# Kernel tuning notes

Measured on AMD Instinct MI355X. Metric: run time of the kernel, lower is better.

Reference implementation:

```python
import jax, jax.numpy as jnp
import numpy as np

B, L, D = 1, 2048, 2048
NH, NKV, HD = 32, 8, 64          # heads, kv heads, head_dim = D // NH
THETA = 50000.0
EPS = 1e-5
SCALE = HD ** -0.5


def _rope(x):
    # traditional (interleaved-pair) RoPE; x: (B, H, L, HD)
    hd = x.shape[-1]
    pos = jnp.arange(x.shape[2], dtype=jnp.float32)
    inv = THETA ** (-jnp.arange(0, hd, 2, dtype=jnp.float32) / hd)
    ang = pos[:, None] * inv[None, :]              # (L, HD/2)
    cos, sin = jnp.cos(ang), jnp.sin(ang)
    x1, x2 = x[..., ::2], x[..., 1::2]
    r1 = x1 * cos - x2 * sin
    r2 = x1 * sin + x2 * cos
    return jnp.stack([r1, r2], axis=-1).reshape(x.shape)


def _rmsnorm(x, w):
    return x * jax.lax.rsqrt(jnp.mean(x * x, axis=-1, keepdims=True) + EPS) * w


def setup_inputs() -> dict:
    key = jax.random.key(0)
    ks = jax.random.split(key, 5)
    x = jax.random.normal(ks[0], (B, L, D), dtype=jnp.float32)
    w_qkv = jax.random.normal(ks[1], (NH * HD + 2 * NKV * HD, D), dtype=jnp.float32) * 0.02
    w_out = jax.random.normal(ks[2], (D, D), dtype=jnp.float32) * 0.02
    q_gamma = 1.0 + 0.02 * jax.random.normal(ks[3], (HD,), dtype=jnp.float32)
    k_gamma = 1.0 + 0.02 * jax.random.normal(ks[4], (HD,), dtype=jnp.float32)
    mask = jnp.tril(jnp.ones((L, L), dtype=bool))   # causal
    return {"x": x, "w_qkv": w_qkv, "w_out": w_out,
            "q_gamma": q_gamma, "k_gamma": k_gamma, "mask": mask}


def reference(x, w_qkv, w_out, q_gamma, k_gamma, mask):
    b, l, d = x.shape
    qkv = x @ w_qkv.T                               # fused QKV proj (no bias)
    q, k, v = jnp.split(qkv, [NH * HD, NH * HD + NKV * HD], axis=-1)
    q = q.reshape(b, l, NH, HD).transpose(0, 2, 1, 3)     # (B,NH,L,HD)
    k = k.reshape(b, l, NKV, HD).transpose(0, 2, 1, 3)    # (B,NKV,L,HD)
    v = v.reshape(b, l, NKV, HD).transpose(0, 2, 1, 3)
    q = _rmsnorm(_rope(q), q_gamma)
    k = _rmsnorm(_rope(k), k_gamma)
    g = NH // NKV                                   # GQA group size
    qg = q.reshape(b, NKV, g, l, HD)
    scores = jnp.einsum('bkgqd,bkld->bkgql', qg, k) * SCALE
    scores = jnp.where(mask, scores, -jnp.inf)
    attn = jax.nn.softmax(scores, axis=-1)
    out = jnp.einsum('bkgql,bkld->bkgqd', attn, v)  # (B,NKV,g,L,HD)
    out = out.reshape(b, NH, l, HD).transpose(0, 2, 1, 3).reshape(b, l, d)
    return out @ w_out.T
```

## Files before the change

kernel.cpp:

```cpp
#include <hip/hip_runtime.h>

using bf16   = __bf16;
using bf16x4 = __bf16 __attribute__((ext_vector_type(4)));
using bf16x8 = __bf16 __attribute__((ext_vector_type(8)));
using f32x4  = float __attribute__((ext_vector_type(4)));
using f32x16 = float __attribute__((ext_vector_type(16)));
using u32x2  = unsigned int __attribute__((ext_vector_type(2)));
using u32x4  = unsigned int __attribute__((ext_vector_type(4)));

#define L_SEQ  2048
#define DMODEL 2048
#define NQH    32
#define NKVH   8
#define HDIM   64
#define QKV_N  3072

#define KVF_HSTRIDE (64 * 4 * 64 * 8)

__device__ __forceinline__ void gload_lds16(const void* g, void* lds) {
  __builtin_amdgcn_global_load_lds((__attribute__((address_space(1))) void*)(g),
                                   (__attribute__((address_space(3))) void*)(lds),
                                   16, 0, 0);
}

__device__ __forceinline__ unsigned pack2(float a, float b) {
  union { bf16 h[2]; unsigned u; } x;
  x.h[0] = (bf16)a; x.h[1] = (bf16)b;
  return x.u;
}

__device__ __forceinline__ bf16x8 make_pfrag(float p0, float p1, float p2, float p3,
                                             float p4, float p5, float p6, float p7,
                                             int hi) {
  const unsigned W0 = pack2(p0, p1);
  const unsigned W1 = pack2(p2, p3);
  const unsigned W2 = pack2(p4, p5);
  const unsigned W3 = pack2(p6, p7);
  u32x4 pw;
#if __has_builtin(__builtin_amdgcn_permlane32_swap)
  {
    using i32x2 = int __attribute__((ext_vector_type(2)));
    const i32x2 r02 = __builtin_amdgcn_permlane32_swap((int)W0, (int)W2, false, false);
    const i32x2 r13 = __builtin_amdgcn_permlane32_swap((int)W1, (int)W3, false, false);
    pw = u32x4{ (unsigned)r02[0], (unsigned)r13[0], (unsigned)r02[1], (unsigned)r13[1] };
  }
#else
  {
    const unsigned X0 = (unsigned)__shfl_xor((int)W0, 32);
    const unsigned X1 = (unsigned)__shfl_xor((int)W1, 32);
    const unsigned X2 = (unsigned)__shfl_xor((int)W2, 32);
    const unsigned X3 = (unsigned)__shfl_xor((int)W3, 32);
    pw = u32x4{ hi ? X2 : W0, hi ? X3 : W1, hi ? W2 : X0, hi ? W3 : X1 };
  }
#endif
  return __builtin_bit_cast(bf16x8, pw);
}

__device__ __forceinline__ int chunk_base(int qi) {
  return (qi < 16) ? qi
       : (qi < 32) ? 16 + 2 * (qi - 16)
       : (qi < 48) ? 48 + 3 * (qi - 32)
                   : 96 + 4 * (qi - 48);
}

#define N4_X  (L_SEQ * DMODEL / 4)
#define N4_WQ (QKV_N * DMODEL / 4)
#define N4_WO (DMODEL * DMODEL / 4)
__global__ void cvt3_f32_bf16(const float* __restrict__ x, const float* __restrict__ wq,
                              const float* __restrict__ wo, bf16* __restrict__ xb,
                              bf16* __restrict__ wqb, bf16* __restrict__ wob) {
  const long stride = (long)gridDim.x * blockDim.x;
  const long ntot = N4_X + N4_WQ + N4_WO;
  for (long i = (long)blockIdx.x * blockDim.x + threadIdx.x; i < ntot; i += stride) {
    const float* src; bf16* dst; long j;
    if (i < N4_X)               { src = x;  dst = xb;  j = i; }
    else if (i < N4_X + N4_WQ)  { src = wq; dst = wqb; j = i - N4_X; }
    else                        { src = wo; dst = wob; j = i - N4_X - N4_WQ; }
    const float4 v = reinterpret_cast<const float4*>(src)[j];
    bf16x4 o = { (bf16)v.x, (bf16)v.y, (bf16)v.z, (bf16)v.w };
    reinterpret_cast<bf16x4*>(dst)[j] = o;
  }
}

template <typename OutT>
__global__ __launch_bounds__(128)
void gemm_bt(const bf16* __restrict__ A, const bf16* __restrict__ B,
             OutT* __restrict__ C, int M, int N, int K) {
  __shared__ bf16 As[128 * 64];
  __shared__ bf16 Bs[64 * 64];
  const int tid = threadIdx.x;
  const int w = tid >> 6, l = tid & 63;
  const int lq = l & 15, lg = l >> 4;
  const long m0 = (long)blockIdx.y * 128;
  const long n0 = (long)blockIdx.x * 64;
  const int ks = K / gridDim.z;
  const int kb = blockIdx.z * ks;
  C += (long)blockIdx.z * M * N;

  const int lrow = l >> 3;
  const int scol = ((l & 7) ^ lrow) << 3;

  f32x4 acc[4][4];
#pragma unroll
  for (int i = 0; i < 4; ++i)
#pragma unroll
    for (int j = 0; j < 4; ++j) acc[i][j] = f32x4{0.f, 0.f, 0.f, 0.f};

  for (int k0 = kb; k0 < kb + ks; k0 += 64) {
#pragma unroll
    for (int i = 0; i < 8; ++i) {
      const int r0 = (i * 2 + w) * 8;
      gload_lds16(A + (m0 + r0 + lrow) * (long)K + k0 + scol, &As[r0 * 64]);
    }
#pragma unroll
    for (int i = 0; i < 4; ++i) {
      const int r0 = (i * 2 + w) * 8;
      gload_lds16(B + (n0 + r0 + lrow) * (long)K + k0 + scol, &Bs[r0 * 64]);
    }
    __syncthreads();
#pragma unroll
    for (int kk = 0; kk < 2; ++kk) {
      bf16x8 af[4], bfr[4];
#pragma unroll
      for (int t = 0; t < 4; ++t) {
        const int rowA = w * 64 + t * 16 + lq;
        const int blkA = (kk * 4 + lg) ^ (rowA & 7);
        af[t] = *reinterpret_cast<const bf16x8*>(&As[rowA * 64 + blkA * 8]);
        const int rowB = t * 16 + lq;
        const int blkB = (kk * 4 + lg) ^ (rowB & 7);
        bfr[t] = *reinterpret_cast<const bf16x8*>(&Bs[rowB * 64 + blkB * 8]);
      }
#pragma unroll
      for (int mt = 0; mt < 4; ++mt)
#pragma unroll
        for (int nt = 0; nt < 4; ++nt)
          acc[mt][nt] = __builtin_amdgcn_mfma_f32_16x16x32_bf16(af[mt], bfr[nt], acc[mt][nt], 0, 0, 0);
    }
    __syncthreads();
  }

#pragma unroll
  for (int mt = 0; mt < 4; ++mt)
#pragma unroll
    for (int r = 0; r < 4; ++r) {
      const long row = m0 + w * 64 + mt * 16 + lg * 4 + r;
#pragma unroll
      for (int nt = 0; nt < 4; ++nt) {
        const long col = n0 + nt * 16 + lq;
        C[row * (long)N + col] = (OutT)acc[mt][nt][r];
      }
    }
}

__global__ __launch_bounds__(256)
void rope_rms(const bf16* __restrict__ pA, const bf16* __restrict__ pB,
              const float* __restrict__ qg, const float* __restrict__ kg,
              bf16* __restrict__ qo, bf16* __restrict__ kfr) {
  const int gid = blockIdx.x * 4 + (threadIdx.x >> 6);
  const int lane = threadIdx.x & 63;
  const int pos = gid / 40;
  const int hh = gid % 40;
  const bool isq = hh < 32;
  const int col = isq ? hh * HDIM : NQH * HDIM + (hh - 32) * HDIM;

  const long idx = (long)pos * QKV_N + col + lane;
  float x = (float)pA[idx] + (float)pB[idx];
  float p = __shfl_xor(x, 1);
  const float fi = (float)(lane & ~1) * (1.0f / 64.0f);
  const float inv = powf(50000.0f, -fi);
  const float ang = (float)pos * inv;
  const float sn = sinf(ang), cs = cosf(ang);
  const float r = (lane & 1) ? (p * sn + x * cs) : (x * cs - p * sn);

  float ss = r * r;
#pragma unroll
  for (int off = 1; off < 64; off <<= 1) ss += __shfl_xor(ss, off);
  const float scl = rsqrtf(ss * (1.0f / 64.0f) + 1e-5f);
  const float g = isq ? qg[lane] : kg[lane];
  const float o = r * scl * g;

  if (isq) {
    qo[(long)pos * DMODEL + hh * HDIM + lane] = (bf16)(o * 0.18033688011112042f);
  } else {
    const int kvh = hh - 32;
    const int d = lane;
    const int lp = (pos & 31) + (((d >> 3) & 1) << 5);
    const long kidx = ((((long)kvh * 64 + (pos >> 5)) * 4 + (d >> 4)) * 64 + lp) * 8 + (d & 7);
    kfr[kidx] = (bf16)o;
  }
}

__global__ __launch_bounds__(256)
void repack_v(const bf16* __restrict__ pA, const bf16* __restrict__ pB,
              bf16* __restrict__ vfr) {
  __shared__ bf16 t[32][72];
  const int kvh = blockIdx.x >> 6;
  const int kb = blockIdx.x & 63;
  const int tid = threadIdx.x;

  {
    const int row = tid >> 3;
    const int cc = (tid & 7) * 8;
    const long goff = (long)(kb * 32 + row) * QKV_N + (NQH * HDIM + NKVH * HDIM) + kvh * HDIM + cc;
    const bf16x8 a = *reinterpret_cast<const bf16x8*>(pA + goff);
    const bf16x8 b = *reinterpret_cast<const bf16x8*>(pB + goff);
    bf16x8 s;
#pragma unroll
    for (int e = 0; e < 8; ++e) s[e] = (bf16)((float)a[e] + (float)b[e]);
    *reinterpret_cast<bf16x8*>(&t[row][cc]) = s;
  }
  __syncthreads();

  const int f = tid >> 6, l = tid & 63;
  const int s = f >> 1, dh = f & 1;
  const int hi = l >> 5, l31 = l & 31;
  union { bf16 b[8]; u32x4 u; } o;
#pragma unroll
  for (int e = 0; e < 8; ++e) o.b[e] = t[s * 16 + hi * 8 + e][dh * 32 + l31];
  bf16* od = vfr + (((long)(kvh * 64 + kb) * 4 + f) * 64 + l) * 8;
  *reinterpret_cast<u32x4*>(od) = o.u;
}

__global__ __launch_bounds__(256)
void flash_attn(const bf16* __restrict__ Q, const bf16* __restrict__ Kfr,
                const bf16* __restrict__ Vfr,
                bf16* __restrict__ po, float* __restrict__ pm, float* __restrict__ pl) {
  const int w = threadIdx.x >> 6, l = threadIdx.x & 63;
  const int lane31 = l & 31, hi = l >> 5;
  const int bb = blockIdx.x;
  const int kvh = bb & 7;
  const int g = bb >> 3;

  int qi, c;
  if (g < 16)      { qi = g;                  c = 0; }
  else if (g < 48) { qi = 16 + ((g - 16) >> 1); c = (g - 16) & 1; }
  else if (g < 96) { qi = 32 + (g - 48) / 3;    c = (g - 48) % 3; }
  else             { qi = 48 + ((g - 96) >> 2); c = (g - 96) & 3; }

  const int h = kvh * 4 + w;
  const int s0 = c * 16;
  const int s1 = min(qi + 1, s0 + 16);
  const int pidx = h * 160 + g;

  const int q0 = qi * 32;
  const int q_abs = q0 + lane31;
  const int l8 = l * 8;

  const bf16* qrow = Q + (long)q_abs * DMODEL + h * HDIM + hi * 8;
  bf16x8 qf[4];
#pragma unroll
  for (int cc = 0; cc < 4; ++cc) qf[cc] = *reinterpret_cast<const bf16x8*>(qrow + cc * 16);

  f32x16 o0, o1;
#pragma unroll
  for (int r = 0; r < 16; ++r) { o0[r] = 0.f; o1[r] = 0.f; }
  float m = -3.0e38f, lsum = 0.f;

  const bf16* kfrh = Kfr + (long)kvh * KVF_HSTRIDE;
  const bf16* vfrh = Vfr + (long)kvh * KVF_HSTRIDE;

  bf16x8 kc0, kc1, kc2, kc3;
  {
    const bf16* kp = kfrh + (long)s0 * 2048 + l8;
    kc0 = *reinterpret_cast<const bf16x8*>(kp);
    kc1 = *reinterpret_cast<const bf16x8*>(kp + 512);
    kc2 = *reinterpret_cast<const bf16x8*>(kp + 1024);
    kc3 = *reinterpret_cast<const bf16x8*>(kp + 1536);
  }

  for (int sti = s0; sti < s1; ++sti) {
    const int kb0 = sti * 32;

    const bf16* vp = vfrh + (long)sti * 2048 + l8;
    const bf16x8 va0 = *reinterpret_cast<const bf16x8*>(vp);
    const bf16x8 vb0 = *reinterpret_cast<const bf16x8*>(vp + 512);
    const bf16x8 va1 = *reinterpret_cast<const bf16x8*>(vp + 1024);
    const bf16x8 vb1 = *reinterpret_cast<const bf16x8*>(vp + 1536);

    const long knoff = (sti + 1 < s1) ? (long)(sti + 1) * 2048 : (long)s0 * 2048;
    const bf16* kp = kfrh + knoff + l8;
    const bf16x8 kn0 = *reinterpret_cast<const bf16x8*>(kp);
    const bf16x8 kn1 = *reinterpret_cast<const bf16x8*>(kp + 512);
    const bf16x8 kn2 = *reinterpret_cast<const bf16x8*>(kp + 1024);
    const bf16x8 kn3 = *reinterpret_cast<const bf16x8*>(kp + 1536);

    f32x16 st;
#pragma unroll
    for (int r = 0; r < 16; ++r) st[r] = 0.f;
    st = __builtin_amdgcn_mfma_f32_32x32x16_bf16(kc0, qf[0], st, 0, 0, 0);
    st = __builtin_amdgcn_mfma_f32_32x32x16_bf16(kc1, qf[1], st, 0, 0, 0);
    st = __builtin_amdgcn_mfma_f32_32x32x16_bf16(kc2, qf[2], st, 0, 0, 0);
    st = __builtin_amdgcn_mfma_f32_32x32x16_bf16(kc3, qf[3], st, 0, 0, 0);

    if (kb0 + 31 > q0) {
#pragma unroll
      for (int r = 0; r < 16; ++r) {
        const int k_abs = kb0 + (r & 3) + 8 * (r >> 2) + 4 * hi;
        if (k_abs > q_abs) st[r] = -3.0e38f;
      }
    }

    float t[8];
#pragma unroll
    for (int r = 0; r < 8; ++r) t[r] = fmaxf(st[r], st[r + 8]);
#pragma unroll
    for (int s = 4; s > 0; s >>= 1)
#pragma unroll
      for (int r = 0; r < 4; ++r) if (r < s) t[r] = fmaxf(t[r], t[r + s]);
    float mx = fmaxf(t[0], __shfl_xor(t[0], 32));

    if (!__all(mx - m <= 8.0f)) {
      const float mn = fmaxf(m, mx);
      const float al = __builtin_amdgcn_exp2f(m - mn);
      m = mn; lsum *= al;
#pragma unroll
      for (int r = 0; r < 16; ++r) { o0[r] *= al; o1[r] *= al; }
    }
    float rs = 0.f;
#pragma unroll
    for (int r = 0; r < 16; ++r) { st[r] = __builtin_amdgcn_exp2f(st[r] - m); rs += st[r]; }
    rs += __shfl_xor(rs, 32);
    lsum += rs;

    {
      const bf16x8 pf0 = make_pfrag(st[0], st[1], st[2], st[3], st[4], st[5], st[6], st[7], hi);
      o0 = __builtin_amdgcn_mfma_f32_32x32x16_bf16(va0, pf0, o0, 0, 0, 0);
      o1 = __builtin_amdgcn_mfma_f32_32x32x16_bf16(vb0, pf0, o1, 0, 0, 0);
      const bf16x8 pf1 = make_pfrag(st[8], st[9], st[10], st[11], st[12], st[13], st[14], st[15], hi);
      o0 = __builtin_amdgcn_mfma_f32_32x32x16_bf16(va1, pf1, o0, 0, 0, 0);
      o1 = __builtin_amdgcn_mfma_f32_32x32x16_bf16(vb1, pf1, o1, 0, 0, 0);
    }

    kc0 = kn0; kc1 = kn1; kc2 = kn2; kc3 = kn3;
  }

  bf16* pbase = po + (long)pidx * 2048 + lane31 * 64;
#pragma unroll
  for (int gg = 0; gg < 4; ++gg) {
    const int d0 = 8 * gg + 4 * hi;
    u32x2 s0v = { pack2(o0[4 * gg + 0], o0[4 * gg + 1]),
                  pack2(o0[4 * gg + 2], o0[4 * gg + 3]) };
    u32x2 s1v = { pack2(o1[4 * gg + 0], o1[4 * gg + 1]),
                  pack2(o1[4 * gg + 2], o1[4 * gg + 3]) };
    *reinterpret_cast<u32x2*>(pbase + d0) = s0v;
    *reinterpret_cast<u32x2*>(pbase + 32 + d0) = s1v;
  }
  if (hi == 0) {
    pm[pidx * 32 + lane31] = m;
    pl[pidx * 32 + lane31] = lsum;
  }
}

__global__ __launch_bounds__(256)
void combine_split(const bf16* __restrict__ po, const float* __restrict__ pm,
                   const float* __restrict__ pl, bf16* __restrict__ ao) {
  const int t = blockIdx.x * 2 + (threadIdx.x >> 7);
  const int tid7 = threadIdx.x & 127;
  const int r = tid7 >> 2;
  const int dc = (tid7 & 3) * 16;
  const int h = t >> 6, qi = t & 63;
  const int nc = 1 + (qi >> 4);
  const int p0 = h * 160 + chunk_base(qi);

  float mv0 = -3e38f, mv1 = -3e38f, mv2 = -3e38f, mv3 = -3e38f;
  float lv0 = 0.f, lv1 = 0.f, lv2 = 0.f, lv3 = 0.f;
  mv0 = pm[(p0 + 0) * 32 + r];              lv0 = pl[(p0 + 0) * 32 + r];
  if (nc > 1) { mv1 = pm[(p0 + 1) * 32 + r]; lv1 = pl[(p0 + 1) * 32 + r]; }
  if (nc > 2) { mv2 = pm[(p0 + 2) * 32 + r]; lv2 = pl[(p0 + 2) * 32 + r]; }
  if (nc > 3) { mv3 = pm[(p0 + 3) * 32 + r]; lv3 = pl[(p0 + 3) * 32 + r]; }
  const float M = fmaxf(fmaxf(mv0, mv1), fmaxf(mv2, mv3));
  const float w0 = __builtin_amdgcn_exp2f(mv0 - M);
  const float w1 = (nc > 1) ? __builtin_amdgcn_exp2f(mv1 - M) : 0.f;
  const float w2 = (nc > 2) ? __builtin_amdgcn_exp2f(mv2 - M) : 0.f;
  const float w3 = (nc > 3) ? __builtin_amdgcn_exp2f(mv3 - M) : 0.f;
  const float invL = 1.0f / (lv0 * w0 + lv1 * w1 + lv2 * w2 + lv3 * w3);

  float acc[16];
#pragma unroll
  for (int j = 0; j < 16; ++j) acc[j] = 0.f;

#pragma unroll
  for (int c = 0; c < 4; ++c) {
    if (c < nc) {
      const float fc = ((c == 0) ? w0 : (c == 1) ? w1 : (c == 2) ? w2 : w3) * invL;
      const bf16* src = po + ((long)(p0 + c) * 2048) + r * 64 + dc;
      const bf16x8 a0 = *reinterpret_cast<const bf16x8*>(src);
      const bf16x8 a1 = *reinterpret_cast<const bf16x8*>(src + 8);
#pragma unroll
      for (int j = 0; j < 8; ++j) {
        acc[j]     += (float)a0[j] * fc;
        acc[8 + j] += (float)a1[j] * fc;
      }
    }
  }

  const long q_abs = (long)qi * 32 + r;
  bf16* od = ao + q_abs * DMODEL + h * HDIM + dc;
  union { bf16 b[16]; u32x4 u[2]; } o;
#pragma unroll
  for (int j = 0; j < 16; ++j) o.b[j] = (bf16)acc[j];
  *reinterpret_cast<u32x4*>(od) = o.u[0];
  *reinterpret_cast<u32x4*>(od + 8) = o.u[1];
}

extern "C" void kernel_launch(void* const* d_in, const int* in_sizes, int n_in,
                              void* d_out, int out_size, void* d_ws, size_t ws_size,
                              hipStream_t stream) {
  const float* x       = (const float*)d_in[0];
  const float* w_qkv   = (const float*)d_in[1];
  const float* w_out   = (const float*)d_in[2];
  const float* q_gamma = (const float*)d_in[3];
  const float* k_gamma = (const float*)d_in[4];

  char* ws = (char*)d_ws;
  bf16* xb    = (bf16*)(ws);
  bf16* wqb   = (bf16*)(ws + (8ul  << 20));
  bf16* wob   = (bf16*)(ws + (20ul << 20));
  bf16* qkvpA = (bf16*)(ws + (28ul << 20));
  bf16* qkvpB = (bf16*)(ws + (40ul << 20));
  bf16* qb    = (bf16*)(ws);
  bf16* kfr   = (bf16*)(ws + (8ul  << 20));
  bf16* vfr   = (bf16*)(ws + (10ul << 20));
  bf16* po    = (bf16*)(ws + (28ul << 20));
  float* pm   = (float*)(ws + (48ul << 20));
  float* pl   = (float*)(ws + (49ul << 20));
  bf16* ao    = (bf16*)(ws + (52ul << 20));
  float* out  = (float*)d_out;

  cvt3_f32_bf16<<<2048, 256, 0, stream>>>(x, w_qkv, w_out, xb, wqb, wob);

  gemm_bt<bf16><<<dim3(QKV_N / 64, L_SEQ / 128, 2), 128, 0, stream>>>(xb, wqb, qkvpA, L_SEQ, QKV_N, DMODEL);

  rope_rms<<<(L_SEQ * 40) / 4, 256, 0, stream>>>(qkvpA, qkvpB, q_gamma, k_gamma, qb, kfr);
  repack_v<<<NKVH * (L_SEQ / 32), 256, 0, stream>>>(qkvpA, qkvpB, vfr);

  flash_attn<<<1280, 256, 0, stream>>>(qb, kfr, vfr, po, pm, pl);
  combine_split<<<1024, 256, 0, stream>>>(po, pm, pl, ao);

  gemm_bt<float><<<dim3(DMODEL / 64, L_SEQ / 128, 1), 128, 0, stream>>>(ao, wob, out, L_SEQ, DMODEL, DMODEL);
}
```

Before: 168.9 us.

## Stage K/V tiles through double-buffered LDS via async global-to-LDS loads

Previously each of the four waves loaded the same K and V fragments straight from global memory into registers. Now the block loads each K/V tile into shared memory once, using async global_load_lds, with double buffering. Each wave then reads its fragments from LDS, which is meant to cut redundant global/L2 traffic by about 4x. The cost is a block-wide barrier every iteration and an LDS read step on the critical path.

```diff
diff --git a/kernel.cpp b/kernel.cpp
--- a/kernel.cpp
+++ b/kernel.cpp
@@ -225,7 +225,10 @@
 void flash_attn(const bf16* __restrict__ Q, const bf16* __restrict__ Kfr,
                 const bf16* __restrict__ Vfr,
                 bf16* __restrict__ po, float* __restrict__ pm, float* __restrict__ pl) {
-  const int w = threadIdx.x >> 6, l = threadIdx.x & 63;
+  __shared__ bf16 Ks[2][2048];
+  __shared__ bf16 Vs[2][2048];
+  const int tid = threadIdx.x;
+  const int w = tid >> 6, l = tid & 63;
   const int lane31 = l & 31, hi = l >> 5;
   const int bb = blockIdx.x;
   const int kvh = bb & 7;
@@ -246,6 +249,9 @@
   const int q_abs = q0 + lane31;
   const int l8 = l * 8;
 
+  const bf16* kfrh = Kfr + (long)kvh * KVF_HSTRIDE;
+  const bf16* vfrh = Vfr + (long)kvh * KVF_HSTRIDE;
+
   const bf16* qrow = Q + (long)q_abs * DMODEL + h * HDIM + hi * 8;
   bf16x8 qf[4];
 #pragma unroll
@@ -256,34 +262,23 @@
   for (int r = 0; r < 16; ++r) { o0[r] = 0.f; o1[r] = 0.f; }
   float m = -3.0e38f, lsum = 0.f;
 
-  const bf16* kfrh = Kfr + (long)kvh * KVF_HSTRIDE;
-  const bf16* vfrh = Vfr + (long)kvh * KVF_HSTRIDE;
-
-  bf16x8 kc0, kc1, kc2, kc3;
-  {
-    const bf16* kp = kfrh + (long)s0 * 2048 + l8;
-    kc0 = *reinterpret_cast<const bf16x8*>(kp);
-    kc1 = *reinterpret_cast<const bf16x8*>(kp + 512);
-    kc2 = *reinterpret_cast<const bf16x8*>(kp + 1024);
-    kc3 = *reinterpret_cast<const bf16x8*>(kp + 1536);
-  }
-
+  gload_lds16(kfrh + (long)s0 * 2048 + tid * 8, &Ks[0][tid * 8]);
+  gload_lds16(vfrh + (long)s0 * 2048 + tid * 8, &Vs[0][tid * 8]);
+  __syncthreads();
+
+  int buf = 0;
   for (int sti = s0; sti < s1; ++sti) {
     const int kb0 = sti * 32;
 
-    const bf16* vp = vfrh + (long)sti * 2048 + l8;
-    const bf16x8 va0 = *reinterpret_cast<const bf16x8*>(vp);
-    const bf16x8 vb0 = *reinterpret_cast<const bf16x8*>(vp + 512);
-    const bf16x8 va1 = *reinterpret_cast<const bf16x8*>(vp + 1024);
-    const bf16x8 vb1 = *reinterpret_cast<const bf16x8*>(vp + 1536);
-
-    const long knoff = (sti + 1 < s1) ? (long)(sti + 1) * 2048 : (long)s0 * 2048;
-    const bf16* kp = kfrh + knoff + l8;
-    const bf16x8 kn0 = *reinterpret_cast<const bf16x8*>(kp);
-    const bf16x8 kn1 = *reinterpret_cast<const bf16x8*>(kp + 512);
-    const bf16x8 kn2 = *reinterpret_cast<const bf16x8*>(kp + 1024);
-    const bf16x8 kn3 = *reinterpret_cast<const bf16x8*>(kp + 1536);
-
+    if (sti + 1 < s1) {
+      gload_lds16(kfrh + (long)(sti + 1) * 2048 + tid * 8, &Ks[buf ^ 1][tid * 8]);
+      gload_lds16(vfrh + (long)(sti + 1) * 2048 + tid * 8, &Vs[buf ^ 1][tid * 8]);
+    }
+
+    const bf16x8 kc0 = *reinterpret_cast<const bf16x8*>(&Ks[buf][l8]);
+    const bf16x8 kc1 = *reinterpret_cast<const bf16x8*>(&Ks[buf][512 + l8]);
+    const bf16x8 kc2 = *reinterpret_cast<const bf16x8*>(&Ks[buf][1024 + l8]);
+    const bf16x8 kc3 = *reinterpret_cast<const bf16x8*>(&Ks[buf][1536 + l8]);
     f32x16 st;
 #pragma unroll
     for (int r = 0; r < 16; ++r) st[r] = 0.f;
@@ -291,6 +286,11 @@
     st = __builtin_amdgcn_mfma_f32_32x32x16_bf16(kc1, qf[1], st, 0, 0, 0);
     st = __builtin_amdgcn_mfma_f32_32x32x16_bf16(kc2, qf[2], st, 0, 0, 0);
     st = __builtin_amdgcn_mfma_f32_32x32x16_bf16(kc3, qf[3], st, 0, 0, 0);
+
+    const bf16x8 va0 = *reinterpret_cast<const bf16x8*>(&Vs[buf][l8]);
+    const bf16x8 vb0 = *reinterpret_cast<const bf16x8*>(&Vs[buf][512 + l8]);
+    const bf16x8 va1 = *reinterpret_cast<const bf16x8*>(&Vs[buf][1024 + l8]);
+    const bf16x8 vb1 = *reinterpret_cast<const bf16x8*>(&Vs[buf][1536 + l8]);
 
     if (kb0 + 31 > q0) {
 #pragma unroll
@@ -331,7 +331,8 @@
       o1 = __builtin_amdgcn_mfma_f32_32x32x16_bf16(vb1, pf1, o1, 0, 0, 0);
     }
 
-    kc0 = kn0; kc1 = kn1; kc2 = kn2; kc3 = kn3;
+    __syncthreads();
+    buf ^= 1;
   }
 
   bf16* pbase = po + (long)pidx * 2048 + lane31 * 64;
```

Result: slower. 172.8 us (+2.3%).

## Process two 32-row query tiles per wave to reuse K/V fragments

Applied to the files above, without the earlier changes.

Each wave in the flash attention kernel now handles 64 query rows, as two 32-row tiles, instead of 32. Every loaded K/V fragment therefore feeds two QK and PV MFMA chains, which halves K/V global traffic per unit of work and halves the grid to 640 blocks. The block order is reversed so the heaviest, most-split causal tiles launch first, and launch_bounds is set to 2 blocks per SM. The combine kernel and the partial-result layout are changed to 64-row chunks. The cost is higher register pressure from four accumulators and fewer blocks to balance the load.

```diff
diff --git a/kernel.cpp b/kernel.cpp
--- a/kernel.cpp
+++ b/kernel.cpp
@@ -56,11 +56,11 @@
   return __builtin_bit_cast(bf16x8, pw);
 }
 
-__device__ __forceinline__ int chunk_base(int qi) {
-  return (qi < 16) ? qi
-       : (qi < 32) ? 16 + 2 * (qi - 16)
-       : (qi < 48) ? 48 + 3 * (qi - 32)
-                   : 96 + 4 * (qi - 48);
+__device__ __forceinline__ int chunk_base64(int Qb) {
+  return (Qb < 8)  ? Qb
+       : (Qb < 16) ? 8  + 2 * (Qb - 8)
+       : (Qb < 24) ? 24 + 3 * (Qb - 16)
+                   : 48 + 4 * (Qb - 24);
 }
 
 #define N4_X  (L_SEQ * DMODEL / 4)
@@ -221,7 +221,7 @@
   *reinterpret_cast<u32x4*>(od) = o.u;
 }
 
-__global__ __launch_bounds__(256)
+__global__ __launch_bounds__(256, 2)
 void flash_attn(const bf16* __restrict__ Q, const bf16* __restrict__ Kfr,
                 const bf16* __restrict__ Vfr,
                 bf16* __restrict__ po, float* __restrict__ pm, float* __restrict__ pl) {
@@ -229,35 +229,40 @@
   const int lane31 = l & 31, hi = l >> 5;
   const int bb = blockIdx.x;
   const int kvh = bb & 7;
-  const int g = bb >> 3;
-
-  int qi, c;
-  if (g < 16)      { qi = g;                  c = 0; }
-  else if (g < 48) { qi = 16 + ((g - 16) >> 1); c = (g - 16) & 1; }
-  else if (g < 96) { qi = 32 + (g - 48) / 3;    c = (g - 48) % 3; }
-  else             { qi = 48 + ((g - 96) >> 2); c = (g - 96) & 3; }
+  const int g = 79 - (bb >> 3);
+
+  int Qb, c;
+  if (g < 8)       { Qb = g;                   c = 0; }
+  else if (g < 24) { Qb = 8 + ((g - 8) >> 1);  c = (g - 8) & 1; }
+  else if (g < 48) { Qb = 16 + (g - 24) / 3;   c = (g - 24) % 3; }
+  else             { Qb = 24 + ((g - 48) >> 2); c = (g - 48) & 3; }
 
   const int h = kvh * 4 + w;
   const int s0 = c * 16;
-  const int s1 = min(qi + 1, s0 + 16);
-  const int pidx = h * 160 + g;
-
-  const int q0 = qi * 32;
-  const int q_abs = q0 + lane31;
+  const int s1 = min(2 * Qb + 2, s0 + 16);
+  const int pidx = h * 80 + g;
+
+  const int q0A = Qb * 64;
+  const int qA = q0A + lane31;
+  const int qB = q0A + 32 + lane31;
   const int l8 = l * 8;
-
-  const bf16* qrow = Q + (long)q_abs * DMODEL + h * HDIM + hi * 8;
-  bf16x8 qf[4];
-#pragma unroll
-  for (int cc = 0; cc < 4; ++cc) qf[cc] = *reinterpret_cast<const bf16x8*>(qrow + cc * 16);
-
-  f32x16 o0, o1;
-#pragma unroll
-  for (int r = 0; r < 16; ++r) { o0[r] = 0.f; o1[r] = 0.f; }
-  float m = -3.0e38f, lsum = 0.f;
 
   const bf16* kfrh = Kfr + (long)kvh * KVF_HSTRIDE;
   const bf16* vfrh = Vfr + (long)kvh * KVF_HSTRIDE;
+
+  const bf16* qrowA = Q + (long)qA * DMODEL + h * HDIM + hi * 8;
+  const bf16* qrowB = Q + (long)qB * DMODEL + h * HDIM + hi * 8;
+  bf16x8 qfA[4], qfB[4];
+#pragma unroll
+  for (int cc = 0; cc < 4; ++cc) {
+    qfA[cc] = *reinterpret_cast<const bf16x8*>(qrowA + cc * 16);
+    qfB[cc] = *reinterpret_cast<const bf16x8*>(qrowB + cc * 16);
+  }
+
+  f32x16 oA0, oA1, oB0, oB1;
+#pragma unroll
+  for (int r = 0; r < 16; ++r) { oA0[r] = 0.f; oA1[r] = 0.f; oB0[r] = 0.f; oB1[r] = 0.f; }
+  float mA = -3.0e38f, lsA = 0.f, mB = -3.0e38f, lsB = 0.f;
 
   bf16x8 kc0, kc1, kc2, kc3;
   {
@@ -284,90 +289,145 @@
     const bf16x8 kn2 = *reinterpret_cast<const bf16x8*>(kp + 1024);
     const bf16x8 kn3 = *reinterpret_cast<const bf16x8*>(kp + 1536);
 
-    f32x16 st;
-#pragma unroll
-    for (int r = 0; r < 16; ++r) st[r] = 0.f;
-    st = __builtin_amdgcn_mfma_f32_32x32x16_bf16(kc0, qf[0], st, 0, 0, 0);
-    st = __builtin_amdgcn_mfma_f32_32x32x16_bf16(kc1, qf[1], st, 0, 0, 0);
-    st = __builtin_amdgcn_mfma_f32_32x32x16_bf16(kc2, qf[2], st, 0, 0, 0);
-    st = __builtin_amdgcn_mfma_f32_32x32x16_bf16(kc3, qf[3], st, 0, 0, 0);
-
-    if (kb0 + 31 > q0) {
-#pragma unroll
-      for (int r = 0; r < 16; ++r) {
-        const int k_abs = kb0 + (r & 3) + 8 * (r >> 2) + 4 * hi;
-        if (k_abs > q_abs) st[r] = -3.0e38f;
-      }
-    }
-
-    float t[8];
-#pragma unroll
-    for (int r = 0; r < 8; ++r) t[r] = fmaxf(st[r], st[r + 8]);
-#pragma unroll
-    for (int s = 4; s > 0; s >>= 1)
-#pragma unroll
-      for (int r = 0; r < 4; ++r) if (r < s) t[r] = fmaxf(t[r], t[r + s]);
-    float mx = fmaxf(t[0], __shfl_xor(t[0], 32));
-
-    if (!__all(mx - m <= 8.0f)) {
-      const float mn = fmaxf(m, mx);
-      const float al = __builtin_amdgcn_exp2f(m - mn);
-      m = mn; lsum *= al;
-#pragma unroll
-      for (int r = 0; r < 16; ++r) { o0[r] *= al; o1[r] *= al; }
-    }
-    float rs = 0.f;
-#pragma unroll
-    for (int r = 0; r < 16; ++r) { st[r] = __builtin_amdgcn_exp2f(st[r] - m); rs += st[r]; }
-    rs += __shfl_xor(rs, 32);
-    lsum += rs;
+    if (kb0 <= q0A + 31) {
+      f32x16 st;
+#pragma unroll
+      for (int r = 0; r < 16; ++r) st[r] = 0.f;
+      st = __builtin_amdgcn_mfma_f32_32x32x16_bf16(kc0, qfA[0], st, 0, 0, 0);
+      st = __builtin_amdgcn_mfma_f32_32x32x16_bf16(kc1, qfA[1], st, 0, 0, 0);
+      st = __builtin_amdgcn_mfma_f32_32x32x16_bf16(kc2, qfA[2], st, 0, 0, 0);
+      st = __builtin_amdgcn_mfma_f32_32x32x16_bf16(kc3, qfA[3], st, 0, 0, 0);
+
+      if (kb0 + 31 > q0A) {
+#pragma unroll
+        for (int r = 0; r < 16; ++r) {
+          const int k_abs = kb0 + (r & 3) + 8 * (r >> 2) + 4 * hi;
+          if (k_abs > qA) st[r] = -3.0e38f;
+        }
+      }
+
+      float t[8];
+#pragma unroll
+      for (int r = 0; r < 8; ++r) t[r] = fmaxf(st[r], st[r + 8]);
+#pragma unroll
+      for (int s = 4; s > 0; s >>= 1)
+#pragma unroll
+        for (int r = 0; r < 4; ++r) if (r < s) t[r] = fmaxf(t[r], t[r + s]);
+      const float mx = fmaxf(t[0], __shfl_xor(t[0], 32));
+
+      if (!__all(mx - mA <= 8.0f)) {
+        const float mn = fmaxf(mA, mx);
+        const float al = __builtin_amdgcn_exp2f(mA - mn);
+        mA = mn; lsA *= al;
+#pragma unroll
+        for (int r = 0; r < 16; ++r) { oA0[r] *= al; oA1[r] *= al; }
+      }
+      float rs = 0.f;
+#pragma unroll
+      for (int r = 0; r < 16; ++r) { st[r] = __builtin_amdgcn_exp2f(st[r] - mA); rs += st[r]; }
+      rs += __shfl_xor(rs, 32);
+      lsA += rs;
+
+      const bf16x8 pf0 = make_pfrag(st[0], st[1], st[2], st[3], st[4], st[5], st[6], st[7], hi);
+      oA0 = __builtin_amdgcn_mfma_f32_32x32x16_bf16(va0, pf0, oA0, 0, 0, 0);
+      oA1 = __builtin_amdgcn_mfma_f32_32x32x16_bf16(vb0, pf0, oA1, 0, 0, 0);
+      const bf16x8 pf1 = make_pfrag(st[8], st[9], st[10], st[11], st[12], st[13], st[14], st[15], hi);
+      oA0 = __builtin_amdgcn_mfma_f32_32x32x16_bf16(va1, pf1, oA0, 0, 0, 0);
+      oA1 = __builtin_amdgcn_mfma_f32_32x32x16_bf16(vb1, pf1, oA1, 0, 0, 0);
+    }
 
     {
+      f32x16 st;
+#pragma unroll
+      for (int r = 0; r < 16; ++r) st[r] = 0.f;
+      st = __builtin_amdgcn_mfma_f32_32x32x16_bf16(kc0, qfB[0], st, 0, 0, 0);
+      st = __builtin_amdgcn_mfma_f32_32x32x16_bf16(kc1, qfB[1], st, 0, 0, 0);
+      st = __builtin_amdgcn_mfma_f32_32x32x16_bf16(kc2, qfB[2], st, 0, 0, 0);
+      st = __builtin_amdgcn_mfma_f32_32x32x16_bf16(kc3, qfB[3], st, 0, 0, 0);
+
+      if (kb0 + 31 > q0A + 32) {
+#pragma unroll
+        for (int r = 0; r < 16; ++r) {
+          const int k_abs = kb0 + (r & 3) + 8 * (r >> 2) + 4 * hi;
+          if (k_abs > qB) st[r] = -3.0e38f;
+        }
+      }
+
+      float t[8];
+#pragma unroll
+      for (int r = 0; r < 8; ++r) t[r] = fmaxf(st[r], st[r + 8]);
+#pragma unroll
+      for (int s = 4; s > 0; s >>= 1)
+#pragma unroll
+        for (int r = 0; r < 4; ++r) if (r < s) t[r] = fmaxf(t[r], t[r + s]);
+      const float mx = fmaxf(t[0], __shfl_xor(t[0], 32));
+
+      if (!__all(mx - mB <= 8.0f)) {
+        const float mn = fmaxf(mB, mx);
+        const float al = __builtin_amdgcn_exp2f(mB - mn);
+        mB = mn; lsB *= al;
+#pragma unroll
+        for (int r = 0; r < 16; ++r) { oB0[r] *= al; oB1[r] *= al; }
+      }
+      float rs = 0.f;
+#pragma unroll
+      for (int r = 0; r < 16; ++r) { st[r] = __builtin_amdgcn_exp2f(st[r] - mB); rs += st[r]; }
+      rs += __shfl_xor(rs, 32);
+      lsB += rs;
+
       const bf16x8 pf0 = make_pfrag(st[0], st[1], st[2], st[3], st[4], st[5], st[6], st[7], hi);
-      o0 = __builtin_amdgcn_mfma_f32_32x32x16_bf16(va0, pf0, o0, 0, 0, 0);
-      o1 = __builtin_amdgcn_mfma_f32_32x32x16_bf16(vb0, pf0, o1, 0, 0, 0);
+      oB0 = __builtin_amdgcn_mfma_f32_32x32x16_bf16(va0, pf0, oB0, 0, 0, 0);
+      oB1 = __builtin_amdgcn_mfma_f32_32x32x16_bf16(vb0, pf0, oB1, 0, 0, 0);
       const bf16x8 pf1 = make_pfrag(st[8], st[9], st[10], st[11], st[12], st[13], st[14], st[15], hi);
-      o0 = __builtin_amdgcn_mfma_f32_32x32x16_bf16(va1, pf1, o0, 0, 0, 0);
-      o1 = __builtin_amdgcn_mfma_f32_32x32x16_bf16(vb1, pf1, o1, 0, 0, 0);
+      oB0 = __builtin_amdgcn_mfma_f32_32x32x16_bf16(va1, pf1, oB0, 0, 0, 0);
+      oB1 = __builtin_amdgcn_mfma_f32_32x32x16_bf16(vb1, pf1, oB1, 0, 0, 0);
     }
 
     kc0 = kn0; kc1 = kn1; kc2 = kn2; kc3 = kn3;
   }
 
-  bf16* pbase = po + (long)pidx * 2048 + lane31 * 64;
+  bf16* pbase = po + (long)pidx * 4096;
 #pragma unroll
   for (int gg = 0; gg < 4; ++gg) {
     const int d0 = 8 * gg + 4 * hi;
-    u32x2 s0v = { pack2(o0[4 * gg + 0], o0[4 * gg + 1]),
-                  pack2(o0[4 * gg + 2], o0[4 * gg + 3]) };
-    u32x2 s1v = { pack2(o1[4 * gg + 0], o1[4 * gg + 1]),
-                  pack2(o1[4 * gg + 2], o1[4 * gg + 3]) };
-    *reinterpret_cast<u32x2*>(pbase + d0) = s0v;
-    *reinterpret_cast<u32x2*>(pbase + 32 + d0) = s1v;
+    u32x2 a0 = { pack2(oA0[4 * gg + 0], oA0[4 * gg + 1]),
+                 pack2(oA0[4 * gg + 2], oA0[4 * gg + 3]) };
+    u32x2 a1 = { pack2(oA1[4 * gg + 0], oA1[4 * gg + 1]),
+                 pack2(oA1[4 * gg + 2], oA1[4 * gg + 3]) };
+    *reinterpret_cast<u32x2*>(pbase + lane31 * 64 + d0) = a0;
+    *reinterpret_cast<u32x2*>(pbase + lane31 * 64 + 32 + d0) = a1;
+    u32x2 b0 = { pack2(oB0[4 * gg + 0], oB0[4 * gg + 1]),
+                 pack2(oB0[4 * gg + 2], oB0[4 * gg + 3]) };
+    u32x2 b1 = { pack2(oB1[4 * gg + 0], oB1[4 * gg + 1]),
+                 pack2(oB1[4 * gg + 2], oB1[4 * gg + 3]) };
+    *reinterpret_cast<u32x2*>(pbase + (32 + lane31) * 64 + d0) = b0;
+    *reinterpret_cast<u32x2*>(pbase + (32 + lane31) * 64 + 32 + d0) = b1;
   }
   if (hi == 0) {
-    pm[pidx * 32 + lane31] = m;
-    pl[pidx * 32 + lane31] = lsum;
+    pm[pidx * 64 + lane31] = mA;
+    pl[pidx * 64 + lane31] = lsA;
+    pm[pidx * 64 + 32 + lane31] = mB;
+    pl[pidx * 64 + 32 + lane31] = lsB;
   }
 }
 
 __global__ __launch_bounds__(256)
 void combine_split(const bf16* __restrict__ po, const float* __restrict__ pm,
                    const float* __restrict__ pl, bf16* __restrict__ ao) {
-  const int t = blockIdx.x * 2 + (threadIdx.x >> 7);
-  const int tid7 = threadIdx.x & 127;
-  const int r = tid7 >> 2;
-  const int dc = (tid7 & 3) * 16;
-  const int h = t >> 6, qi = t & 63;
-  const int nc = 1 + (qi >> 4);
-  const int p0 = h * 160 + chunk_base(qi);
+  const int t = blockIdx.x;
+  const int tid = threadIdx.x;
+  const int r = tid >> 2;
+  const int dc = (tid & 3) * 16;
+  const int h = t >> 5, Qb = t & 31;
+  const int nc = (Qb < 8) ? 1 : (Qb < 16) ? 2 : (Qb < 24) ? 3 : 4;
+  const int p0 = h * 80 + chunk_base64(Qb);
 
   float mv0 = -3e38f, mv1 = -3e38f, mv2 = -3e38f, mv3 = -3e38f;
   float lv0 = 0.f, lv1 = 0.f, lv2 = 0.f, lv3 = 0.f;
-  mv0 = pm[(p0 + 0) * 32 + r];              lv0 = pl[(p0 + 0) * 32 + r];
-  if (nc > 1) { mv1 = pm[(p0 + 1) * 32 + r]; lv1 = pl[(p0 + 1) * 32 + r]; }
-  if (nc > 2) { mv2 = pm[(p0 + 2) * 32 + r]; lv2 = pl[(p0 + 2) * 32 + r]; }
-  if (nc > 3) { mv3 = pm[(p0 + 3) * 32 + r]; lv3 = pl[(p0 + 3) * 32 + r]; }
+  mv0 = pm[(p0 + 0) * 64 + r];              lv0 = pl[(p0 + 0) * 64 + r];
+  if (nc > 1) { mv1 = pm[(p0 + 1) * 64 + r]; lv1 = pl[(p0 + 1) * 64 + r]; }
+  if (nc > 2) { mv2 = pm[(p0 + 2) * 64 + r]; lv2 = pl[(p0 + 2) * 64 + r]; }
+  if (nc > 3) { mv3 = pm[(p0 + 3) * 64 + r]; lv3 = pl[(p0 + 3) * 64 + r]; }
   const float M = fmaxf(fmaxf(mv0, mv1), fmaxf(mv2, mv3));
   const float w0 = __builtin_amdgcn_exp2f(mv0 - M);
   const float w1 = (nc > 1) ? __builtin_amdgcn_exp2f(mv1 - M) : 0.f;
@@ -383,7 +443,7 @@
   for (int c = 0; c < 4; ++c) {
     if (c < nc) {
       const float fc = ((c == 0) ? w0 : (c == 1) ? w1 : (c == 2) ? w2 : w3) * invL;
-      const bf16* src = po + ((long)(p0 + c) * 2048) + r * 64 + dc;
+      const bf16* src = po + ((long)(p0 + c) * 4096) + r * 64 + dc;
       const bf16x8 a0 = *reinterpret_cast<const bf16x8*>(src);
       const bf16x8 a1 = *reinterpret_cast<const bf16x8*>(src + 8);
 #pragma unroll
@@ -394,7 +454,7 @@
     }
   }
 
-  const long q_abs = (long)qi * 32 + r;
+  const long q_abs = (long)Qb * 64 + r;
   bf16* od = ao + q_abs * DMODEL + h * HDIM + dc;
   union { bf16 b[16]; u32x4 u[2]; } o;
 #pragma unroll
@@ -434,7 +494,7 @@
   rope_rms<<<(L_SEQ * 40) / 4, 256, 0, stream>>>(qkvpA, qkvpB, q_gamma, k_gamma, qb, kfr);
   repack_v<<<NKVH * (L_SEQ / 32), 256, 0, stream>>>(qkvpA, qkvpB, vfr);
 
-  flash_attn<<<1280, 256, 0, stream>>>(qb, kfr, vfr, po, pm, pl);
+  flash_attn<<<640, 256, 0, stream>>>(qb, kfr, vfr, po, pm, pl);
   combine_split<<<1024, 256, 0, stream>>>(po, pm, pl, ao);
 
   gemm_bt<float><<<dim3(DMODEL / 64, L_SEQ / 128, 1), 128, 0, stream>>>(ao, wob, out, L_SEQ, DMODEL, DMODEL);
```

New measurement: 171.6 us. No clear change (+1.6%).
